# Kernel tuning notes

Measured on AMD Instinct MI355X. Metric: run time of the kernel, lower is better.

The kernel has to match this reference:

```python
import jax, jax.numpy as jnp
import numpy as np

STRIDE = 1
PADDING = 1
DILATION = 1


def setup_inputs() -> dict:
    key = jax.random.key(0)
    k1, k2, k3 = jax.random.split(key, 3)
    b_i, b_j, c, h, w = 32, 1, 128, 32, 32
    oc, kh, kw = 128, 3, 3
    x = jax.random.normal(k1, (b_i, b_j, c, h, w), dtype=jnp.float32)
    weight = jax.random.normal(k2, (b_i, oc, c, kh, kw), dtype=jnp.float32) * 0.05
    bias = jax.random.normal(k3, (b_i, b_j, oc), dtype=jnp.float32) * 0.05
    return {"x": x, "weight": weight, "bias": bias}


def reference(x, weight, bias):
    # x: [b_i, b_j, c, h, w]; weight: [b_i, oc, c, kh, kw]; bias: [b_i, b_j, oc]
    b_i, b_j, c, h, w = x.shape
    oc, kh, kw = weight.shape[1], weight.shape[3], weight.shape[4]
    # fold per-sample dim into channels, run one grouped conv with groups=b_i
    xr = jnp.transpose(x, (1, 0, 2, 3, 4)).reshape(b_j, b_i * c, h, w)
    wr = weight.reshape(b_i * oc, c, kh, kw)
    out = jax.lax.conv_general_dilated(
        xr, wr,
        window_strides=(STRIDE, STRIDE),
        padding=[(PADDING, PADDING), (PADDING, PADDING)],
        rhs_dilation=(DILATION, DILATION),
        dimension_numbers=("NCHW", "OIHW", "NCHW"),
        feature_group_count=b_i,
    )  # [b_j, b_i*oc, H, W]
    H, W = out.shape[-2], out.shape[-1]
    out = out.reshape(b_j, b_i, oc, H, W).transpose(1, 0, 2, 3, 4)  # [b_i, b_j, oc, H, W]
    out = out + bias[:, :, :, None, None]
    return out
```

## Files before the change

### kernel.cpp

```cpp
#include <hip/hip_runtime.h>

typedef unsigned short u16;
typedef unsigned int u32;
typedef __attribute__((ext_vector_type(2))) unsigned int u32x2;
typedef __attribute__((ext_vector_type(8))) short bf16x8;
typedef __attribute__((ext_vector_type(4))) float f32x4;

#define CIN 128
#define OC 128
#define NP 1024
#define KTOT 1152
#define NSTEP 18
#define BK 64

__device__ __forceinline__ u16 f2bf(float f) {
  unsigned b = __builtin_bit_cast(unsigned, f);
  b += 0x7fffu + ((b >> 16) & 1u);
  return (u16)(b >> 16);
}

__global__ void wcvt_kernel(const float* __restrict__ w, u16* __restrict__ wbf) {
  __shared__ u16 lds[KTOT];
  const int blk = blockIdx.x;
  const int t = threadIdx.x;
  const float* src = w + (size_t)blk * KTOT;
  u16* dst = wbf + (size_t)blk * KTOT;
#pragma unroll
  for (int e = 0; e < 9; ++e) {
    int idx = t + 128 * e;
    lds[idx] = f2bf(src[idx]);
  }
  __syncthreads();
#pragma unroll
  for (int e = 0; e < 9; ++e) {
    int o = t + 128 * e;
    dst[o] = lds[t * 9 + e];
  }
}

__global__ __launch_bounds__(256, 3) void conv_mfma(
    const float* __restrict__ x,
    const u16* __restrict__ wbf,
    const float* __restrict__ bias,
    float* __restrict__ out) {
  __shared__ u16 Xs[4 * 34 * 128];
  __shared__ u16 Asw[OC * BK];

  const int wg = (int)blockIdx.x;
  const int swz = (wg & 7) * 64 + (wg >> 3);
  const int i  = swz >> 4;
  const int pt = swz & 15;
  const int p0 = pt * 64;
  const int tid = (int)threadIdx.x;
  const int lane = tid & 63;
  const int wid = tid >> 6;
  const int wm = wid >> 1;
  const int wn = wid & 1;

  const float* xi = x + (size_t)i * CIN * NP;
  const u16*   wi = wbf + (size_t)i * OC * KTOT;

  const int arow = tid >> 1;
  const int kh = tid & 1;
  const u16* abase = wi + arow * KTOT + kh * 32;

  bf16x8 ar[4];

#define LOADA(step) do {                                        \
    const u16* _a = abase + (step) * BK;                        \
    _Pragma("unroll")                                           \
    for (int e = 0; e < 4; ++e) ar[e] = *(const bf16x8*)(_a + e * 8); \
  } while (0)

#define STOREA() do {                                           \
    _Pragma("unroll")                                           \
    for (int e = 0; e < 4; ++e) {                               \
      int _slot = (kh * 4 + e) ^ (arow & 7);                    \
      *(bf16x8*)(&Asw[arow * BK + _slot * 8]) = ar[e];          \
    }                                                           \
  } while (0)

  {
    const int xx = tid & 31;
    const int cg = tid >> 5;
    const int col = xx + 1;
    const int csw = col & 7;
#pragma unroll
    for (int r = 0; r < 4; ++r) {
      const int yr = 2 * pt - 1 + r;
      float v[16];
      if ((unsigned)yr < 32u) {
        const float* src = xi + (size_t)(cg * 16) * NP + yr * 32 + xx;
#pragma unroll
        for (int j = 0; j < 16; ++j) v[j] = src[(size_t)j * NP];
      } else {
#pragma unroll
        for (int j = 0; j < 16; ++j) v[j] = 0.f;
      }
      u32 pk[8];
#pragma unroll
      for (int m = 0; m < 8; ++m)
        pk[m] = (u32)f2bf(v[2 * m]) | ((u32)f2bf(v[2 * m + 1]) << 16);
#pragma unroll
      for (int q = 0; q < 4; ++q) {
        const int cslot = cg * 2 + (q >> 1);
        const int idx = ((r * 34 + col) * 16 + (cslot ^ csw)) * 8 + (q & 1) * 4;
        *(u32x2*)(&Xs[idx]) = (u32x2){pk[2 * q], pk[2 * q + 1]};
      }
    }
    if (tid < 128) {
      const int r = tid >> 5;
      const int hc = ((tid >> 4) & 1) ? 33 : 0;
      const int s = tid & 15;
      const int idx = ((r * 34 + hc) * 16 + (s ^ (hc & 7))) * 8;
      *(bf16x8*)(&Xs[idx]) = (bf16x8){0, 0, 0, 0, 0, 0, 0, 0};
    }
  }

  f32x4 acc[4][2];
#pragma unroll
  for (int mi = 0; mi < 4; ++mi)
#pragma unroll
    for (int ni = 0; ni < 2; ++ni)
      acc[mi][ni] = (f32x4){0.f, 0.f, 0.f, 0.f};

  const int cb0 = (lane & 15) + 1;
  const int lhi = lane >> 4;

  LOADA(0);
  STOREA();
  __syncthreads();

#pragma unroll
  for (int step = 0; step < NSTEP; ++step) {
    const int rs = step >> 1;
    const int r3 = rs / 3;
    const int dy = r3 - 1;
    const int dx = (rs - r3 * 3) - 1;
    const int c0s = (step & 1) * 8;
    const int rw = (wn + 1 + dy) * 34;

    if (step + 1 < NSTEP) LOADA(step + 1);

    __builtin_amdgcn_s_setprio(1);
#pragma unroll
    for (int kkk = 0; kkk < 2; ++kkk) {
      bf16x8 af[4], bfr[2];
#pragma unroll
      for (int mi = 0; mi < 4; ++mi) {
        int row = wm * 64 + mi * 16 + (lane & 15);
        int slot = (kkk * 4 + lhi) ^ (row & 7);
        af[mi] = *(const bf16x8*)(&Asw[row * BK + slot * 8]);
      }
#pragma unroll
      for (int ni = 0; ni < 2; ++ni) {
        const int col = cb0 + ni * 16 + dx;
        const int cslot = c0s + kkk * 4 + lhi;
        const int idx = ((rw + col) * 16 + (cslot ^ (col & 7))) * 8;
        bfr[ni] = *(const bf16x8*)(&Xs[idx]);
      }
#pragma unroll
      for (int mi = 0; mi < 4; ++mi)
#pragma unroll
        for (int ni = 0; ni < 2; ++ni)
          acc[mi][ni] = __builtin_amdgcn_mfma_f32_16x16x32_bf16(
              af[mi], bfr[ni], acc[mi][ni], 0, 0, 0);
    }
    __builtin_amdgcn_s_setprio(0);

    if (step + 1 < NSTEP) {
      __syncthreads();
      STOREA();
      __syncthreads();
    }
  }

  const int row0 = (lane >> 4) * 4;
  const int coln = lane & 15;
#pragma unroll
  for (int mi = 0; mi < 4; ++mi) {
    int oc = wm * 64 + mi * 16 + row0;
#pragma unroll
    for (int jj = 0; jj < 4; ++jj) {
      float bv = bias[i * OC + oc + jj];
      float* orow = out + ((size_t)i * OC + oc + jj) * NP;
#pragma unroll
      for (int ni = 0; ni < 2; ++ni) {
        int pg = p0 + wn * 32 + ni * 16 + coln;
        orow[pg] = acc[mi][ni][jj] + bv;
      }
    }
  }
#undef LOADA
#undef STOREA
}

extern "C" void kernel_launch(void* const* d_in, const int* in_sizes, int n_in,
                              void* d_out, int out_size, void* d_ws, size_t ws_size,
                              hipStream_t stream) {
  const float* x    = (const float*)d_in[0];
  const float* w    = (const float*)d_in[1];
  const float* bias = (const float*)d_in[2];
  float* out = (float*)d_out;
  u16* wbf = (u16*)d_ws;

  wcvt_kernel<<<dim3(32 * OC), dim3(128), 0, stream>>>(w, wbf);
  conv_mfma<<<dim3(512), dim3(256), 0, stream>>>(x, wbf, bias, out);
}
```

Before: 30.36 us.

## Load weight fragments directly from global into registers, drop LDS staging

Weight A-fragments are now loaded directly from global memory into MFMA register layout, double-buffered in registers across K steps. This removes the Asw shared buffer and the two barriers per step that staging it required. Each wave now reads its weight rows from global (L2/L1) itself, so the two waves sharing the same rows fetch them twice, and register pressure goes up. Launch bounds drop to 2 blocks per SIMD to make room.

```diff
diff --git a/kernel.cpp b/kernel.cpp
--- a/kernel.cpp
+++ b/kernel.cpp
@@ -38,13 +38,12 @@
   }
 }
 
-__global__ __launch_bounds__(256, 3) void conv_mfma(
+__global__ __launch_bounds__(256, 2) void conv_mfma(
     const float* __restrict__ x,
     const u16* __restrict__ wbf,
     const float* __restrict__ bias,
     float* __restrict__ out) {
   __shared__ u16 Xs[4 * 34 * 128];
-  __shared__ u16 Asw[OC * BK];
 
   const int wg = (int)blockIdx.x;
   const int swz = (wg & 7) * 64 + (wg >> 3);
@@ -60,25 +59,21 @@
   const float* xi = x + (size_t)i * CIN * NP;
   const u16*   wi = wbf + (size_t)i * OC * KTOT;
 
-  const int arow = tid >> 1;
-  const int kh = tid & 1;
-  const u16* abase = wi + arow * KTOT + kh * 32;
+  const int lhi = lane >> 4;
+  const u16* agbase = wi + (size_t)(wm * 64 + (lane & 15)) * KTOT + lhi * 8;
 
-  bf16x8 ar[4];
-
-#define LOADA(step) do {                                        \
-    const u16* _a = abase + (step) * BK;                        \
+#define LOADG(dst, step) do {                                   \
+    const u16* _g = agbase + (step) * BK;                       \
     _Pragma("unroll")                                           \
-    for (int e = 0; e < 4; ++e) ar[e] = *(const bf16x8*)(_a + e * 8); \
+    for (int _kk = 0; _kk < 2; ++_kk)                           \
+      _Pragma("unroll")                                         \
+      for (int _mi = 0; _mi < 4; ++_mi)                         \
+        dst[_kk * 4 + _mi] =                                    \
+            *(const bf16x8*)(_g + _mi * 16 * KTOT + _kk * 32);  \
   } while (0)
 
-#define STOREA() do {                                           \
-    _Pragma("unroll")                                           \
-    for (int e = 0; e < 4; ++e) {                               \
-      int _slot = (kh * 4 + e) ^ (arow & 7);                    \
-      *(bf16x8*)(&Asw[arow * BK + _slot * 8]) = ar[e];          \
-    }                                                           \
-  } while (0)
+  bf16x8 a_cur[8], a_nxt[8];
+  LOADG(a_cur, 0);
 
   {
     const int xx = tid & 31;
@@ -125,10 +120,7 @@
       acc[mi][ni] = (f32x4){0.f, 0.f, 0.f, 0.f};
 
   const int cb0 = (lane & 15) + 1;
-  const int lhi = lane >> 4;
 
-  LOADA(0);
-  STOREA();
   __syncthreads();
 
 #pragma unroll
@@ -140,18 +132,12 @@
     const int c0s = (step & 1) * 8;
     const int rw = (wn + 1 + dy) * 34;
 
-    if (step + 1 < NSTEP) LOADA(step + 1);
+    if (step + 1 < NSTEP) LOADG(a_nxt, step + 1);
 
     __builtin_amdgcn_s_setprio(1);
 #pragma unroll
     for (int kkk = 0; kkk < 2; ++kkk) {
-      bf16x8 af[4], bfr[2];
-#pragma unroll
-      for (int mi = 0; mi < 4; ++mi) {
-        int row = wm * 64 + mi * 16 + (lane & 15);
-        int slot = (kkk * 4 + lhi) ^ (row & 7);
-        af[mi] = *(const bf16x8*)(&Asw[row * BK + slot * 8]);
-      }
+      bf16x8 bfr[2];
 #pragma unroll
       for (int ni = 0; ni < 2; ++ni) {
         const int col = cb0 + ni * 16 + dx;
@@ -164,14 +150,13 @@
 #pragma unroll
         for (int ni = 0; ni < 2; ++ni)
           acc[mi][ni] = __builtin_amdgcn_mfma_f32_16x16x32_bf16(
-              af[mi], bfr[ni], acc[mi][ni], 0, 0, 0);
+              a_cur[kkk * 4 + mi], bfr[ni], acc[mi][ni], 0, 0, 0);
     }
     __builtin_amdgcn_s_setprio(0);
 
     if (step + 1 < NSTEP) {
-      __syncthreads();
-      STOREA();
-      __syncthreads();
+#pragma unroll
+      for (int e = 0; e < 8; ++e) a_cur[e] = a_nxt[e];
     }
   }
 
@@ -191,8 +176,7 @@
       }
     }
   }
-#undef LOADA
-#undef STOREA
+#undef LOADG
 }
 
 extern "C" void kernel_launch(void* const* d_in, const int* in_sizes, int n_in,
```

Result: slower. 50.50 us (+66.3%).
